# Kernel tuning notes

Hardware: AMD Instinct MI355X
Metric: run time of the kernel (lower is better)

## Reference

```python
import jax, jax.numpy as jnp
import numpy as np

B, CIN, COUT, SDIM, RES, K = 8, 512, 512, 512, 64, 3
AFF_SCALE = 1.0 / np.sqrt(SDIM)          # LinearAct: 1/sqrt(in_features)
CONV_SCALE = 1.0 / np.sqrt(CIN * K * K)  # ModulatedConv2d: 1/sqrt(in*k*k)
LRELU_GAIN = np.sqrt(2.0)                # bias_act 'lrelu' default gain


def setup_inputs() -> dict:
    key = jax.random.key(0)
    k = jax.random.split(key, 5)
    x = jax.random.normal(k[0], (B, CIN, RES, RES), dtype=jnp.float32)
    w = jax.random.normal(k[1], (B, SDIM), dtype=jnp.float32)
    noise = jax.random.normal(k[2], (B, 1, RES, RES), dtype=jnp.float32)
    affine_w = jax.random.normal(k[3], (CIN, SDIM), dtype=jnp.float32)
    affine_b = jnp.ones((CIN,), dtype=jnp.float32)          # bias.data.fill_(1.0)
    conv_w = jax.random.normal(k[4], (COUT, CIN, K, K), dtype=jnp.float32)
    noise_scale = jnp.asarray(0.1, dtype=jnp.float32)        # InjectNoise.scale (nonzero for a meaningful test)
    bias = jnp.zeros((COUT,), dtype=jnp.float32)
    return {"x": x, "w": w, "noise": noise, "affine_w": affine_w,
            "affine_b": affine_b, "conv_w": conv_w,
            "noise_scale": noise_scale, "bias": bias}


def reference(x, w, noise, affine_w, affine_b, conv_w, noise_scale, bias):
    # affine (LinearAct, act='linear'): style = w @ (W*scale)^T + b
    style = jnp.einsum('bs,cs->bc', w, affine_w * AFF_SCALE) + affine_b  # [B, CIN]

    # modulate + demodulate: per-sample weight [B, COUT, CIN, K, K]
    wt = conv_w[None] * style[:, None, :, None, None] * CONV_SCALE
    d = jax.lax.rsqrt(jnp.sum(wt * wt, axis=(2, 3, 4), keepdims=True) + 1e-8)
    wt = wt * d

    # grouped conv (groups=B) == per-sample conv; flip_weight=True -> plain correlation
    def conv_one(xi, wi):
        return jax.lax.conv_general_dilated(
            xi[None], wi, window_strides=(1, 1), padding=[(1, 1), (1, 1)],
            dimension_numbers=('NCHW', 'OIHW', 'NCHW'))[0]

    y = jax.vmap(conv_one)(x, wt)  # [B, COUT, RES, RES]

    # noise -> bias -> lrelu(0.2) * sqrt(2)
    y = y + noise * noise_scale
    y = jax.nn.leaky_relu(y + bias[None, :, None, None], 0.2) * LRELU_GAIN
    return y
```

## Files before the change

### kernel.cpp

```cpp
#include <hip/hip_runtime.h>
#include <hip/hip_bf16.h>

typedef unsigned short u16;

#define BATCH 8
#define CIN 512
#define COUT 512
#define SDIM 512
#define RES 64
#define PIX (RES * RES)

__device__ __constant__ static const float kAffScale  = 0.04419417382415922f;
__device__ __constant__ static const float kConvScale = 0.014731391274719742f;
__device__ __constant__ static const float kGain      = 1.4142135623730951f;

typedef __bf16 bf16x8 __attribute__((ext_vector_type(8)));
typedef float  f32x4  __attribute__((ext_vector_type(4)));

__global__ void style_k(const float* __restrict__ w, const float* __restrict__ aw,
                        const float* __restrict__ ab, float* __restrict__ style,
                        float* __restrict__ zbuf) {
  int tid = blockIdx.x * 256 + threadIdx.x;
  if (blockIdx.x == 0 && threadIdx.x < 64) zbuf[threadIdx.x] = 0.0f;
  int b = tid >> 9, c = tid & 511;
  const float* wp = w + b * SDIM;
  const float* ap = aw + c * SDIM;
  float s = 0.0f;
  for (int k = 0; k < SDIM; ++k) s += wp[k] * ap[k];
  style[tid] = s * kAffScale + ab[c];
}

__global__ void cw2_k(const float* __restrict__ cw, float* __restrict__ cw2) {
  int tid = blockIdx.x * 256 + threadIdx.x;
  const float* p = cw + tid * 9;
  float s = 0.0f;
  #pragma unroll
  for (int t = 0; t < 9; ++t) { float v = p[t]; s += v * v; }
  cw2[tid] = s;
}

__global__ void fac_k(const float* __restrict__ style, const float* __restrict__ cw2,
                      float* __restrict__ fac) {
  int wid  = blockIdx.x * 4 + (threadIdx.x >> 6);
  int lane = threadIdx.x & 63;
  int b = wid >> 9, o = wid & 511;
  const float* st = style + b * CIN;
  const float* c2 = cw2 + o * CIN;
  float s = 0.0f;
  for (int i = lane; i < CIN; i += 64) { float sv = st[i]; s += sv * sv * c2[i]; }
  #pragma unroll
  for (int off = 32; off; off >>= 1) s += __shfl_xor(s, off);
  if (lane == 0) {
    float d = rsqrtf(s * kConvScale * kConvScale + 1e-8f);
    fac[wid] = d * kConvScale;
  }
}

__global__ void wcast_k(const float* __restrict__ cw, u16* __restrict__ wb) {
  int tid = blockIdx.x * 256 + threadIdx.x;
  int o = tid >> 9, i = tid & 511;
  const float* p = cw + tid * 9;
  #pragma unroll
  for (int t = 0; t < 9; ++t) {
    __hip_bfloat16 h = __float2bfloat16(p[t]);
    wb[(t * COUT + o) * CIN + i] = *(u16*)&h;
  }
}

__global__ void modx_k(const float* __restrict__ x, const float* __restrict__ style,
                       u16* __restrict__ xs) {
  __shared__ float t[64][65];
  int b  = blockIdx.z;
  int it = blockIdx.y * 64;
  int pt = blockIdx.x * 64;
  int tp = threadIdx.x & 63;
  int tr = threadIdx.x >> 6;
  for (int r = tr; r < 64; r += 4) {
    int i = it + r;
    t[r][tp] = x[(b * CIN + i) * PIX + pt + tp] * style[b * CIN + i];
  }
  __syncthreads();
  for (int r = tr; r < 64; r += 4) {
    __hip_bfloat16 h = __float2bfloat16(t[tp][r]);
    xs[(size_t)(b * PIX + pt + r) * CIN + it + tp] = *(u16*)&h;
  }
}

__launch_bounds__(512, 2)
__global__ void gemm_k(const u16* __restrict__ wb, const u16* __restrict__ xs,
                       const float* __restrict__ fac, const float* __restrict__ noise,
                       const float* __restrict__ nscale_p, const float* __restrict__ bias,
                       const float* __restrict__ zbuf, float* __restrict__ y) {
  __shared__ __align__(16) u16 Abuf[4][256 * 32];
  __shared__ __align__(16) u16 Bbuf[4][256 * 32];

  const int tid = threadIdx.x;
  const int bid = blockIdx.x;
  const int swz = (bid & 7) * 32 + (bid >> 3);
  const int mt = swz >> 7;
  const int nt = swz & 127;
  const int b  = nt >> 4;
  const int pimg  = (nt & 15) * 256;
  const int hbase = pimg >> 6;

  const int lane = tid & 63;
  const int wv = tid >> 6;
  const int wm = wv >> 2;
  const int wn = wv & 3;
  const int l15 = lane & 15, l4 = lane >> 4;

  const int sg = ((tid & 3) ^ ((tid >> 3) & 3)) * 8;
  int offA[2], hrB[2], wwB[2];
  #pragma unroll
  for (int p = 0; p < 2; ++p) {
    int row = (p * 512 + tid) >> 2;
    offA[p] = (mt * 256 + row) * CIN + sg;
    hrB[p]  = hbase + (row >> 6);
    wwB[p]  = row & 63;
  }

  f32x4 acc[8][4];
  #pragma unroll
  for (int i = 0; i < 8; ++i)
    #pragma unroll
    for (int j = 0; j < 4; ++j) acc[i][j] = (f32x4){0.f, 0.f, 0.f, 0.f};

  auto stage = [&](int kk, int buf) {
    const int tap = kk >> 4;
    const int i0  = (kk & 15) << 5;
    const int dy  = tap < 3 ? -1 : (tap < 6 ? 0 : 1);
    const int dx  = (tap % 3) - 1;
    const size_t tapoff = (size_t)tap * (COUT * CIN) + i0;
    #pragma unroll
    for (int p = 0; p < 2; ++p) {
      int c = p * 512 + tid;
      const u16* src = wb + tapoff + offA[p];
      __builtin_amdgcn_global_load_lds(
          (const __attribute__((address_space(1))) void*)src,
          (__attribute__((address_space(3))) void*)(&Abuf[buf][c * 8]), 16, 0, 0);
    }
    #pragma unroll
    for (int p = 0; p < 2; ++p) {
      int c = p * 512 + tid;
      int hh = hrB[p] + dy, ww = wwB[p] + dx;
      const u16* src = ((unsigned)hh < 64u && (unsigned)ww < 64u)
          ? xs + ((size_t)(b * PIX + hh * 64 + ww) * CIN + i0 + sg)
          : (const u16*)zbuf;
      __builtin_amdgcn_global_load_lds(
          (const __attribute__((address_space(1))) void*)src,
          (__attribute__((address_space(3))) void*)(&Bbuf[buf][c * 8]), 16, 0, 0);
    }
  };

  stage(0, 0); stage(1, 1); stage(2, 2);
  asm volatile("s_waitcnt vmcnt(8)" ::: "memory");
  __builtin_amdgcn_s_barrier();

  const int slr = (l4 ^ ((l15 >> 1) & 3)) * 8;

  for (int kk = 0; kk < 144; ++kk) {
    const int buf = kk & 3;
    if (kk < 141) stage(kk + 3, (kk + 3) & 3);

    const u16* Ab = &Abuf[buf][0];
    const u16* Bb = &Bbuf[buf][0];
    bf16x8 af[8], bfr[4];
    #pragma unroll
    for (int mi = 0; mi < 8; ++mi) {
      int r = wm * 128 + mi * 16 + l15;
      af[mi] = *(const bf16x8*)&Ab[r * 32 + slr];
    }
    #pragma unroll
    for (int ni = 0; ni < 4; ++ni) {
      int r = wn * 64 + ni * 16 + l15;
      bfr[ni] = *(const bf16x8*)&Bb[r * 32 + slr];
    }
    #pragma unroll
    for (int mi = 0; mi < 8; ++mi)
      #pragma unroll
      for (int ni = 0; ni < 4; ++ni)
        acc[mi][ni] = __builtin_amdgcn_mfma_f32_16x16x32_bf16(af[mi], bfr[ni],
                                                              acc[mi][ni], 0, 0, 0);
    if (kk < 143) {
      const int rem = 143 - kk;
      if (rem > 2)       asm volatile("s_waitcnt vmcnt(8)" ::: "memory");
      else if (rem == 2) asm volatile("s_waitcnt vmcnt(4)" ::: "memory");
      else               asm volatile("s_waitcnt vmcnt(0)" ::: "memory");
      asm volatile("s_waitcnt lgkmcnt(0)" ::: "memory");
      __builtin_amdgcn_s_barrier();
    }
  }

  const float ns = nscale_p[0];
  float nz[4];
  #pragma unroll
  for (int ni = 0; ni < 4; ++ni) {
    int pix = pimg + wn * 64 + ni * 16 + l15;
    nz[ni] = noise[b * PIX + pix] * ns;
  }
  #pragma unroll
  for (int mi = 0; mi < 8; ++mi) {
    int o = mt * 256 + wm * 128 + mi * 16 + l4 * 4;
    f32x4 fv = *(const f32x4*)&fac[b * COUT + o];
    f32x4 bv = *(const f32x4*)&bias[o];
    #pragma unroll
    for (int r = 0; r < 4; ++r) {
      float* yp = y + (size_t)(b * COUT + o + r) * PIX + pimg + wn * 64 + l15;
      #pragma unroll
      for (int ni = 0; ni < 4; ++ni) {
        float v = acc[mi][ni][r] * fv[r] + nz[ni] + bv[r];
        v = (v > 0.0f ? v : 0.2f * v) * kGain;
        yp[ni * 16] = v;
      }
    }
  }
}

extern "C" void kernel_launch(void* const* d_in, const int* in_sizes, int n_in,
                              void* d_out, int out_size, void* d_ws, size_t ws_size,
                              hipStream_t stream) {
  const float* x      = (const float*)d_in[0];
  const float* w      = (const float*)d_in[1];
  const float* noise  = (const float*)d_in[2];
  const float* aff_w  = (const float*)d_in[3];
  const float* aff_b  = (const float*)d_in[4];
  const float* conv_w = (const float*)d_in[5];
  const float* nscale = (const float*)d_in[6];
  const float* bias   = (const float*)d_in[7];
  float* y = (float*)d_out;

  char* ws = (char*)d_ws;
  float* style = (float*)(ws);
  float* fac   = (float*)(ws + 16384);
  float* cw2   = (float*)(ws + 32768);
  float* zbuf  = (float*)(ws + 1081344);
  u16*   wb    = (u16*)(ws + 1081600);
  u16*   xs    = (u16*)(ws + 5800192);

  style_k<<<16, 256, 0, stream>>>(w, aff_w, aff_b, style, zbuf);
  cw2_k<<<1024, 256, 0, stream>>>(conv_w, cw2);
  fac_k<<<1024, 256, 0, stream>>>(style, cw2, fac);
  wcast_k<<<1024, 256, 0, stream>>>(conv_w, wb);
  modx_k<<<dim3(64, 8, 8), 256, 0, stream>>>(x, style, xs);
  gemm_k<<<256, 512, 0, stream>>>(wb, xs, fac, noise, nscale, bias, zbuf, y);
}
```

Baseline: 232.3 us.

## Restructure GEMM main loop into 64-wide K tiles with interleaved half-tile prefetch

The conv GEMM main loop moves from 144 iterations of K=32 with a 4-deep LDS ring to 72 iterations of K=64 with double buffering. Each iteration is split into four phases that interleave LDS fragment reads, issue of the next half-tile's global-to-LDS loads, and MFMA bursts wrapped in s_setprio and sched_barrier. The goal is to overlap memory traffic with matrix math more finely and keep fewer fragments live in registers. It adds more barriers per iteration, and the final iterations issue wrapped redundant prefetches (ktx wraps past NKT), which costs extra loads.

Measured after the change: 200.0 us. -13.9%, faster.

```diff
diff --git a/kernel.cpp b/kernel.cpp
--- a/kernel.cpp
+++ b/kernel.cpp
@@ -9,6 +9,7 @@
 #define SDIM 512
 #define RES 64
 #define PIX (RES * RES)
+#define NKT 72
 
 __device__ __constant__ static const float kAffScale  = 0.04419417382415922f;
 __device__ __constant__ static const float kConvScale = 0.014731391274719742f;
@@ -91,8 +92,8 @@
                        const float* __restrict__ fac, const float* __restrict__ noise,
                        const float* __restrict__ nscale_p, const float* __restrict__ bias,
                        const float* __restrict__ zbuf, float* __restrict__ y) {
-  __shared__ __align__(16) u16 Abuf[4][256 * 32];
-  __shared__ __align__(16) u16 Bbuf[4][256 * 32];
+  __shared__ __align__(16) u16 Abuf[2][16384];
+  __shared__ __align__(16) u16 Bbuf[2][16384];
 
   const int tid = threadIdx.x;
   const int bid = blockIdx.x;
@@ -108,88 +109,139 @@
   const int wm = wv >> 2;
   const int wn = wv & 3;
   const int l15 = lane & 15, l4 = lane >> 4;
-
-  const int sg = ((tid & 3) ^ ((tid >> 3) & 3)) * 8;
-  int offA[2], hrB[2], wwB[2];
+  const int slot = (l4 ^ ((l15 >> 1) & 3)) * 8;
+
+  const int sg8 = (((tid & 3) ^ ((tid >> 3) & 3)) << 3);
+  size_t offA[2]; int hr[2], wc[2];
   #pragma unroll
   for (int p = 0; p < 2; ++p) {
     int row = (p * 512 + tid) >> 2;
-    offA[p] = (mt * 256 + row) * CIN + sg;
-    hrB[p]  = hbase + (row >> 6);
-    wwB[p]  = row & 63;
-  }
-
-  f32x4 acc[8][4];
-  #pragma unroll
-  for (int i = 0; i < 8; ++i)
-    #pragma unroll
-    for (int j = 0; j < 4; ++j) acc[i][j] = (f32x4){0.f, 0.f, 0.f, 0.f};
-
-  auto stage = [&](int kk, int buf) {
-    const int tap = kk >> 4;
-    const int i0  = (kk & 15) << 5;
-    const int dy  = tap < 3 ? -1 : (tap < 6 ? 0 : 1);
-    const int dx  = (tap % 3) - 1;
-    const size_t tapoff = (size_t)tap * (COUT * CIN) + i0;
+    offA[p] = (size_t)(mt * 256 + row) * CIN + sg8;
+    hr[p] = hbase + (row >> 6);
+    wc[p] = row & 63;
+  }
+
+  auto stA = [&](int ktx, int kh) {
+    if (ktx >= NKT) ktx -= NKT;
+    const int tap = ktx >> 3;
+    const int i0  = (ktx & 7) << 6;
+    const int d   = ktx & 1;
+    const u16* basep = wb + (size_t)tap * (COUT * CIN) + i0 + kh * 32;
     #pragma unroll
     for (int p = 0; p < 2; ++p) {
-      int c = p * 512 + tid;
-      const u16* src = wb + tapoff + offA[p];
+      const u16* src = basep + offA[p];
       __builtin_amdgcn_global_load_lds(
           (const __attribute__((address_space(1))) void*)src,
-          (__attribute__((address_space(3))) void*)(&Abuf[buf][c * 8]), 16, 0, 0);
+          (__attribute__((address_space(3))) void*)(&Abuf[d][kh * 8192 + (p * 512 + tid) * 8]),
+          16, 0, 0);
     }
+  };
+  auto stB = [&](int ktx, int kh) {
+    if (ktx >= NKT) ktx -= NKT;
+    const int tap = ktx >> 3;
+    const int i0  = (ktx & 7) << 6;
+    const int dy  = tap < 3 ? -1 : (tap < 6 ? 0 : 1);
+    const int dx  = (tap - (tap < 3 ? 0 : (tap < 6 ? 3 : 6))) - 1;
+    const int d   = ktx & 1;
     #pragma unroll
     for (int p = 0; p < 2; ++p) {
-      int c = p * 512 + tid;
-      int hh = hrB[p] + dy, ww = wwB[p] + dx;
+      int hh = hr[p] + dy, ww = wc[p] + dx;
       const u16* src = ((unsigned)hh < 64u && (unsigned)ww < 64u)
-          ? xs + ((size_t)(b * PIX + hh * 64 + ww) * CIN + i0 + sg)
+          ? xs + ((size_t)(b * PIX + hh * 64 + ww) * CIN + i0 + kh * 32 + sg8)
           : (const u16*)zbuf;
       __builtin_amdgcn_global_load_lds(
           (const __attribute__((address_space(1))) void*)src,
-          (__attribute__((address_space(3))) void*)(&Bbuf[buf][c * 8]), 16, 0, 0);
+          (__attribute__((address_space(3))) void*)(&Bbuf[d][kh * 8192 + (p * 512 + tid) * 8]),
+          16, 0, 0);
     }
   };
 
-  stage(0, 0); stage(1, 1); stage(2, 2);
+  f32x4 acc[8][4];
+  #pragma unroll
+  for (int i = 0; i < 8; ++i)
+    #pragma unroll
+    for (int j = 0; j < 4; ++j) acc[i][j] = (f32x4){0.f, 0.f, 0.f, 0.f};
+
+  stA(0, 0); stB(0, 0); stA(0, 1); stB(0, 1); stA(1, 0); stB(1, 0);
   asm volatile("s_waitcnt vmcnt(8)" ::: "memory");
   __builtin_amdgcn_s_barrier();
 
-  const int slr = (l4 ^ ((l15 >> 1) & 3)) * 8;
-
-  for (int kk = 0; kk < 144; ++kk) {
-    const int buf = kk & 3;
-    if (kk < 141) stage(kk + 3, (kk + 3) & 3);
-
-    const u16* Ab = &Abuf[buf][0];
-    const u16* Bb = &Bbuf[buf][0];
-    bf16x8 af[8], bfr[4];
-    #pragma unroll
-    for (int mi = 0; mi < 8; ++mi) {
-      int r = wm * 128 + mi * 16 + l15;
-      af[mi] = *(const bf16x8*)&Ab[r * 32 + slr];
-    }
-    #pragma unroll
-    for (int ni = 0; ni < 4; ++ni) {
-      int r = wn * 64 + ni * 16 + l15;
-      bfr[ni] = *(const bf16x8*)&Bb[r * 32 + slr];
-    }
-    #pragma unroll
-    for (int mi = 0; mi < 8; ++mi)
-      #pragma unroll
-      for (int ni = 0; ni < 4; ++ni)
-        acc[mi][ni] = __builtin_amdgcn_mfma_f32_16x16x32_bf16(af[mi], bfr[ni],
-                                                              acc[mi][ni], 0, 0, 0);
-    if (kk < 143) {
-      const int rem = 143 - kk;
-      if (rem > 2)       asm volatile("s_waitcnt vmcnt(8)" ::: "memory");
-      else if (rem == 2) asm volatile("s_waitcnt vmcnt(4)" ::: "memory");
-      else               asm volatile("s_waitcnt vmcnt(0)" ::: "memory");
-      asm volatile("s_waitcnt lgkmcnt(0)" ::: "memory");
-      __builtin_amdgcn_s_barrier();
-    }
-  }
+#define LDA(mi, kh) (*(const bf16x8*)&Ab[(kh) * 8192 + (wm * 128 + (mi) * 16 + l15) * 32 + slot])
+#define LDB(ni, kh) (*(const bf16x8*)&Bb[(kh) * 8192 + (wn * 64 + (ni) * 16 + l15) * 32 + slot])
+
+  for (int kt = 0; kt < NKT; ++kt) {
+    const u16* Ab = &Abuf[kt & 1][0];
+    const u16* Bb = &Bbuf[kt & 1][0];
+    bf16x8 bfr[4], af[4];
+
+    #pragma unroll
+    for (int ni = 0; ni < 4; ++ni) bfr[ni] = LDB(ni, 0);
+    #pragma unroll
+    for (int j = 0; j < 4; ++j) af[j] = LDA(j, 0);
+    stA(kt + 1, 1);
+    __builtin_amdgcn_s_barrier();
+    asm volatile("s_waitcnt lgkmcnt(0)" ::: "memory");
+    __builtin_amdgcn_sched_barrier(0);
+    __builtin_amdgcn_s_setprio(1);
+    #pragma unroll
+    for (int j = 0; j < 4; ++j)
+      #pragma unroll
+      for (int ni = 0; ni < 4; ++ni)
+        acc[j][ni] = __builtin_amdgcn_mfma_f32_16x16x32_bf16(af[j], bfr[ni], acc[j][ni], 0, 0, 0);
+    __builtin_amdgcn_s_setprio(0);
+    __builtin_amdgcn_s_barrier();
+
+    #pragma unroll
+    for (int j = 0; j < 4; ++j) af[j] = LDA(4 + j, 0);
+    stB(kt + 1, 1);
+    __builtin_amdgcn_s_barrier();
+    asm volatile("s_waitcnt lgkmcnt(0)" ::: "memory");
+    __builtin_amdgcn_sched_barrier(0);
+    __builtin_amdgcn_s_setprio(1);
+    #pragma unroll
+    for (int j = 0; j < 4; ++j)
+      #pragma unroll
+      for (int ni = 0; ni < 4; ++ni)
+        acc[4 + j][ni] = __builtin_amdgcn_mfma_f32_16x16x32_bf16(af[j], bfr[ni], acc[4 + j][ni], 0, 0, 0);
+    __builtin_amdgcn_s_setprio(0);
+    asm volatile("s_waitcnt vmcnt(8)" ::: "memory");
+    __builtin_amdgcn_s_barrier();
+
+    #pragma unroll
+    for (int ni = 0; ni < 4; ++ni) bfr[ni] = LDB(ni, 1);
+    #pragma unroll
+    for (int j = 0; j < 4; ++j) af[j] = LDA(j, 1);
+    stA(kt + 2, 0);
+    __builtin_amdgcn_s_barrier();
+    asm volatile("s_waitcnt lgkmcnt(0)" ::: "memory");
+    __builtin_amdgcn_sched_barrier(0);
+    __builtin_amdgcn_s_setprio(1);
+    #pragma unroll
+    for (int j = 0; j < 4; ++j)
+      #pragma unroll
+      for (int ni = 0; ni < 4; ++ni)
+        acc[j][ni] = __builtin_amdgcn_mfma_f32_16x16x32_bf16(af[j], bfr[ni], acc[j][ni], 0, 0, 0);
+    __builtin_amdgcn_s_setprio(0);
+    __builtin_amdgcn_s_barrier();
+
+    #pragma unroll
+    for (int j = 0; j < 4; ++j) af[j] = LDA(4 + j, 1);
+    stB(kt + 2, 0);
+    __builtin_amdgcn_s_barrier();
+    asm volatile("s_waitcnt lgkmcnt(0)" ::: "memory");
+    __builtin_amdgcn_sched_barrier(0);
+    __builtin_amdgcn_s_setprio(1);
+    #pragma unroll
+    for (int j = 0; j < 4; ++j)
+      #pragma unroll
+      for (int ni = 0; ni < 4; ++ni)
+        acc[4 + j][ni] = __builtin_amdgcn_mfma_f32_16x16x32_bf16(af[j], bfr[ni], acc[4 + j][ni], 0, 0, 0);
+    __builtin_amdgcn_s_setprio(0);
+    asm volatile("s_waitcnt vmcnt(8)" ::: "memory");
+    __builtin_amdgcn_s_barrier();
+  }
+#undef LDA
+#undef LDB
 
   const float ns = nscale_p[0];
   float nz[4];
```
